# Performance work log

Measured on AMD Instinct MI355X. Metric: run time of the kernel, lower is better.

## Reference

```python
import jax, jax.numpy as jnp
import numpy as np

EPS = 1e-5

def _layer_norm(x, gamma, beta):
    mu = jnp.mean(x, axis=-1, keepdims=True)
    var = jnp.var(x, axis=-1, keepdims=True)
    return (x - mu) * jax.lax.rsqrt(var + EPS) * gamma + beta

def setup_inputs() -> dict:
    key = jax.random.key(0)
    ks = jax.random.split(key, 4)
    B, T, D, H = 16, 2048, 1024, 1024
    s_in = 1.0 / np.sqrt(D)
    return {
        "x": jax.random.normal(ks[0], (B, T, D), dtype=jnp.float32),
        "c": jnp.zeros((B, H), dtype=jnp.float32),
        "W_lt": jax.random.uniform(ks[1], (H, D), jnp.float32, -s_in, s_in),
        "W_g": jax.random.uniform(ks[2], (2 * H, D), jnp.float32, -s_in, s_in),
        "b_g": jnp.zeros((2 * H,), dtype=jnp.float32),
        "gamma_g": jnp.ones((2 * H,), dtype=jnp.float32),
        "beta_g": jnp.zeros((2 * H,), dtype=jnp.float32),
        "gamma_a": jnp.ones((H,), dtype=jnp.float32),
        "beta_a": jnp.zeros((H,), dtype=jnp.float32),
    }

def reference(x, c, W_lt, W_g, b_g, gamma_g, beta_g, gamma_a, beta_a):
    H = W_lt.shape[0]
    # x: [B,T,D]
    x_tilde = jnp.einsum("btd,hd->bth", x, W_lt)            # [B,T,H]
    gate = jax.nn.sigmoid(_layer_norm(jnp.einsum("btd,gd->btg", x, W_g) + b_g, gamma_g, beta_g))
    f = gate[:, :, :H]                                        # forget gate [B,T,H]
    r = gate[:, :, H:]                                        # reset gate  [B,T,H]
    new_data = (1.0 - f) * x_tilde

    def step(c_prev, ft_nd):
        f_t, nd_t = ft_nd
        c_t = f_t * c_prev + nd_t
        return c_t, c_t

    # scan over time: move T to leading axis
    c_final, all_c = jax.lax.scan(step, c, (jnp.swapaxes(f, 0, 1), jnp.swapaxes(new_data, 0, 1)))
    all_c = jnp.swapaxes(all_c, 0, 1)                         # [B,T,H]
    h = r * jax.nn.sigmoid(_layer_norm(all_c, gamma_a, beta_a)) + (1.0 - r) * x
    return (h, c_final)
```

## Files before the change

### kernel.cpp

```cpp
#include <hip/hip_runtime.h>
#include <stdint.h>

typedef unsigned short u16;
typedef u16 us8 __attribute__((ext_vector_type(8)));
typedef uint32_t u32x8 __attribute__((ext_vector_type(8)));
typedef __bf16 bf16x8 __attribute__((ext_vector_type(8)));
typedef float f32x4 __attribute__((ext_vector_type(4)));

#define BB 16
#define TT 2048
#define HH 1024
#define MM 32768
#define NN 3072
#define KK 1024
#define NT 16

__device__ __forceinline__ float b2f(u16 u) {
    union { uint32_t i; float f; } v; v.i = ((uint32_t)u) << 16; return v.f;
}
__device__ __forceinline__ u16 f2b(float f) {
    union { uint32_t i; float f; } v; v.f = f;
    uint32_t r = v.i + 0x7fffu + ((v.i >> 16) & 1u);
    return (u16)(r >> 16);
}
__device__ __forceinline__ float sigm(float z) {
    return 1.f / (1.f + __expf(-z));
}
__device__ __forceinline__ void load_lds16(const u16* g, u16* l) {
    __builtin_amdgcn_global_load_lds(
        (const __attribute__((address_space(1))) void*)g,
        (__attribute__((address_space(3))) void*)l, 16, 0, 0);
}
__device__ __forceinline__ f32x4 mf(bf16x8 a, bf16x8 b, f32x4 c) {
    return __builtin_amdgcn_mfma_f32_16x16x32_bf16(a, b, c, 0, 0, 0);
}

__global__ __launch_bounds__(256) void k_cvt(const float* __restrict__ x,
                                             const float* __restrict__ wlt,
                                             const float* __restrict__ wg,
                                             u16* __restrict__ xb,
                                             u16* __restrict__ wb) {
    long i = (long)(blockIdx.x * 256 + threadIdx.x) * 8;
    const float* s;
    u16* o;
    if (i < 33554432L) { s = x + i; o = xb + i; }
    else {
        long j = i - 33554432L;
        s = (j < 1048576L) ? (wlt + j) : (wg + (j - 1048576L));
        o = wb + j;
    }
    float4 a = *(const float4*)(s);
    float4 b = *(const float4*)(s + 4);
    us8 r;
    r[0] = f2b(a.x); r[1] = f2b(a.y); r[2] = f2b(a.z); r[3] = f2b(a.w);
    r[4] = f2b(b.x); r[5] = f2b(b.y); r[6] = f2b(b.z); r[7] = f2b(b.w);
    *(us8*)o = r;
}

__global__ __launch_bounds__(512, 2) void k_gemm(const u16* __restrict__ A,
                                                 const u16* __restrict__ W,
                                                 u16* __restrict__ Y) {
    __shared__ u16 As[2 * 16384];
    __shared__ u16 Bs[2 * 16384];
    const int tid = threadIdx.x;
    const int lane = tid & 63;
    const int w = tid >> 6;
    const int wm = w >> 2;
    const int wn = w & 3;
    const int q = lane >> 4;
    const int l16 = lane & 15;
    const int bx = blockIdx.x;
    const int by = blockIdx.y;

    const int slog = ((tid & 7) ^ ((tid >> 3) & 7)) << 3;
    const u16* aS = A + (size_t)(by * 256 + (tid >> 3)) * KK + slog;
    const u16* bS = W + (size_t)(bx * 256 + ((tid >> 8) << 6) + ((tid >> 3) & 31)) * KK + slog;
    u16* aD = As + w * 512;
    u16* bD = Bs + w * 512;

    load_lds16(aS,                aD);
    load_lds16(aS + 128 * KK,     aD + 4096);
    load_lds16(aS + 64 * KK,      aD + 8192);
    load_lds16(aS + 192 * KK,     aD + 12288);
    load_lds16(bS,                bD);
    load_lds16(bS + 128 * KK,     bD + 4096);
    load_lds16(bS + 32 * KK,      bD + 8192);
    load_lds16(bS + 160 * KK,     bD + 12288);
    load_lds16(aS + 64,           aD + 16384);
    load_lds16(aS + 64 + 128*KK,  aD + 16384 + 4096);
    load_lds16(aS + 64 + 64*KK,   aD + 16384 + 8192);
    load_lds16(aS + 64 + 192*KK,  aD + 16384 + 12288);
    load_lds16(bS + 64,           bD + 16384);
    load_lds16(bS + 64 + 128*KK,  bD + 16384 + 4096);
    load_lds16(bS + 64 + 32*KK,   bD + 16384 + 8192);
    load_lds16(bS + 64 + 160*KK,  bD + 16384 + 12288);

    const int key = l16 & 7;
    const int sA0 = ((q ^ key) << 3);
    const int sA1 = (((q ^ key) ^ 4) << 3);
    const int aB0 = wm * 4096 + l16 * 64 + sA0;
    const int aB1 = wm * 4096 + l16 * 64 + sA1;
    const int bB0 = wn * 2048 + l16 * 64 + sA0;
    const int bB1 = wn * 2048 + l16 * 64 + sA1;

    f32x4 zero = {0.f, 0.f, 0.f, 0.f};
    f32x4 acc[8][4];
#pragma unroll
    for (int i = 0; i < 8; ++i)
#pragma unroll
        for (int j = 0; j < 4; ++j) acc[i][j] = zero;
    bf16x8 aR[4][2], bR[4][2];

    asm volatile("s_waitcnt vmcnt(8)" ::: "memory");
    __builtin_amdgcn_sched_barrier(0);
    __builtin_amdgcn_s_barrier();
    asm volatile("" ::: "memory");

    for (int kt = 0; kt < NT; ++kt) {
        const int cb = (kt & 1) << 14;
        const int kc = (kt + 2) << 6;
#pragma unroll
        for (int i = 0; i < 4; ++i) {
            aR[i][0] = *(const bf16x8*)&As[cb + i * 1024 + aB0];
            aR[i][1] = *(const bf16x8*)&As[cb + i * 1024 + aB1];
        }
#pragma unroll
        for (int f = 0; f < 4; ++f) {
            bR[f][0] = *(const bf16x8*)&Bs[cb + (f >> 1) * 8192 + (f & 1) * 1024 + bB0];
            bR[f][1] = *(const bf16x8*)&Bs[cb + (f >> 1) * 8192 + (f & 1) * 1024 + bB1];
        }
        asm volatile("" ::: "memory");
        __builtin_amdgcn_s_barrier();
        asm volatile("s_waitcnt lgkmcnt(0)" ::: "memory");
        __builtin_amdgcn_sched_barrier(0);
        __builtin_amdgcn_s_setprio(1);
#pragma unroll
        for (int i = 0; i < 4; ++i)
#pragma unroll
            for (int f = 0; f < 2; ++f) {
                acc[i][f] = mf(aR[i][0], bR[f][0], acc[i][f]);
                acc[i][f] = mf(aR[i][1], bR[f][1], acc[i][f]);
            }
        __builtin_amdgcn_s_setprio(0);
        asm volatile("" ::: "memory");
        __builtin_amdgcn_s_barrier();
        asm volatile("" ::: "memory");
        if (kt < NT - 2) {
            load_lds16(aS + kc,            aD + cb);
            load_lds16(aS + kc + 128*KK,   aD + cb + 4096);
            load_lds16(bS + kc,            bD + cb);
            load_lds16(bS + kc + 128*KK,   bD + cb + 4096);
            load_lds16(bS + kc + 32*KK,    bD + cb + 8192);
            load_lds16(bS + kc + 160*KK,   bD + cb + 12288);
        }
        asm volatile("" ::: "memory");
        __builtin_amdgcn_s_barrier();
        __builtin_amdgcn_s_setprio(1);
#pragma unroll
        for (int i = 0; i < 4; ++i)
#pragma unroll
            for (int f = 2; f < 4; ++f) {
                acc[i][f] = mf(aR[i][0], bR[f][0], acc[i][f]);
                acc[i][f] = mf(aR[i][1], bR[f][1], acc[i][f]);
            }
        __builtin_amdgcn_s_setprio(0);
        asm volatile("" ::: "memory");
        __builtin_amdgcn_s_barrier();
        asm volatile("" ::: "memory");
#pragma unroll
        for (int i = 0; i < 4; ++i) {
            aR[i][0] = *(const bf16x8*)&As[cb + 8192 + i * 1024 + aB0];
            aR[i][1] = *(const bf16x8*)&As[cb + 8192 + i * 1024 + aB1];
        }
        asm volatile("" ::: "memory");
        __builtin_amdgcn_s_barrier();
        asm volatile("s_waitcnt lgkmcnt(0)" ::: "memory");
        __builtin_amdgcn_sched_barrier(0);
        __builtin_amdgcn_s_setprio(1);
#pragma unroll
        for (int i = 0; i < 4; ++i)
#pragma unroll
            for (int f = 0; f < 2; ++f) {
                acc[4 + i][f] = mf(aR[i][0], bR[f][0], acc[4 + i][f]);
                acc[4 + i][f] = mf(aR[i][1], bR[f][1], acc[4 + i][f]);
            }
        __builtin_amdgcn_s_setprio(0);
        asm volatile("" ::: "memory");
        __builtin_amdgcn_s_barrier();
        asm volatile("" ::: "memory");
        if (kt < NT - 2) {
            load_lds16(aS + kc + 64*KK,    aD + cb + 8192);
            load_lds16(aS + kc + 192*KK,   aD + cb + 12288);
        }
        asm volatile("" ::: "memory");
        __builtin_amdgcn_s_barrier();
        __builtin_amdgcn_s_setprio(1);
#pragma unroll
        for (int i = 0; i < 4; ++i)
#pragma unroll
            for (int f = 2; f < 4; ++f) {
                acc[4 + i][f] = mf(aR[i][0], bR[f][0], acc[4 + i][f]);
                acc[4 + i][f] = mf(aR[i][1], bR[f][1], acc[4 + i][f]);
            }
        __builtin_amdgcn_s_setprio(0);
        if (kt < NT - 2) { asm volatile("s_waitcnt vmcnt(8)" ::: "memory"); }
        else             { asm volatile("s_waitcnt vmcnt(0)" ::: "memory"); }
        __builtin_amdgcn_sched_barrier(0);
        __builtin_amdgcn_s_barrier();
        asm volatile("" ::: "memory");
    }

#pragma unroll
    for (int fm = 0; fm < 8; ++fm) {
#pragma unroll
        for (int rg = 0; rg < 4; ++rg) {
            const int row = by * 256 + wm * 128 + fm * 16 + q * 4 + rg;
            u16* yp = Y + (size_t)row * NN + bx * 256 + wn * 64 + l16;
#pragma unroll
            for (int fn = 0; fn < 4; ++fn) yp[fn * 16] = f2b(acc[fm][fn][rg]);
        }
    }
}

__global__ __launch_bounds__(256) void k_lnsig(const u16* __restrict__ Y,
                                               const float* __restrict__ bg,
                                               const float* __restrict__ gg,
                                               const float* __restrict__ bt,
                                               uint32_t* __restrict__ FN,
                                               u16* __restrict__ R) {
    const int row = blockIdx.x;
    const int t = threadIdx.x;
    const u16* yr = Y + (size_t)row * 3072;
    us8 gv = *(const us8*)(yr + 1024 + t * 8);
    float z[8];
    float s = 0.f, s2 = 0.f;
#pragma unroll
    for (int k = 0; k < 8; k++) {
        z[k] = b2f(gv[k]) + bg[t * 8 + k];
        s += z[k];
        s2 += z[k] * z[k];
    }
#pragma unroll
    for (int m = 1; m < 64; m <<= 1) {
        s += __shfl_xor(s, m);
        s2 += __shfl_xor(s2, m);
    }
    __shared__ float red[8];
    if ((t & 63) == 0) { red[t >> 6] = s; red[(t >> 6) + 4] = s2; }
    __syncthreads();
    s = red[0] + red[1] + red[2] + red[3];
    s2 = red[4] + red[5] + red[6] + red[7];
    const float mu = s * (1.f / 2048.f);
    const float inv = rsqrtf(s2 * (1.f / 2048.f) - mu * mu + 1e-5f);
    float gate[8];
#pragma unroll
    for (int k = 0; k < 8; k++)
        gate[k] = sigm((z[k] - mu) * inv * gg[t * 8 + k] + bt[t * 8 + k]);
    if (t < 128) {
        us8 xt = *(const us8*)(yr + t * 8);
        u32x8 fn;
#pragma unroll
        for (int k = 0; k < 8; k++) {
            u16 fb = f2b(gate[k]);
            u16 nb = f2b((1.f - gate[k]) * b2f(xt[k]));
            fn[k] = (uint32_t)fb | ((uint32_t)nb << 16);
        }
        *(u32x8*)(FN + (size_t)row * 1024 + t * 8) = fn;
    } else {
        us8 ro;
#pragma unroll
        for (int k = 0; k < 8; k++) ro[k] = f2b(gate[k]);
        *(us8*)(R + (size_t)row * 1024 + (t - 128) * 8) = ro;
    }
}

__global__ __launch_bounds__(256) void k_scan1(const uint32_t* __restrict__ FN,
                                               float2* __restrict__ agg) {
    int u = blockIdx.x * 256 + threadIdx.x;
    int h2 = u & 511;
    int chunk = (u >> 9) & 31;
    int b = u >> 14;
    size_t base = (size_t)(b * 2048 + chunk * 64) * 1024 + h2 * 2;
    float F0 = 1.f, N0 = 0.f, F1 = 1.f, N1 = 0.f;
#pragma unroll 4
    for (int i = 0; i < 64; i++) {
        uint2 v = *(const uint2*)(FN + base + (size_t)i * 1024);
        float f0 = b2f((u16)(v.x & 0xffffu)), n0 = b2f((u16)(v.x >> 16));
        float f1 = b2f((u16)(v.y & 0xffffu)), n1 = b2f((u16)(v.y >> 16));
        N0 = fmaf(f0, N0, n0); F0 *= f0;
        N1 = fmaf(f1, N1, n1); F1 *= f1;
    }
    float4 o = {F0, N0, F1, N1};
    *(float4*)&agg[(size_t)(b * 32 + chunk) * 1024 + h2 * 2] = o;
}

__global__ __launch_bounds__(256) void k_scan2(const float2* __restrict__ agg,
                                               const float* __restrict__ c0,
                                               float* __restrict__ P) {
    int u = blockIdx.x * 256 + threadIdx.x;
    int b = u >> 10, h = u & 1023;
    float c = c0[u];
#pragma unroll 4
    for (int k = 0; k < 32; k++) {
        size_t idx = (size_t)(b * 32 + k) * 1024 + h;
        P[idx] = c;
        float2 fn = agg[idx];
        c = fmaf(fn.x, c, fn.y);
    }
}

__global__ __launch_bounds__(512) void k_scanout(const uint32_t* __restrict__ FN,
                                                 const float* __restrict__ P,
                                                 const u16* __restrict__ R,
                                                 const u16* __restrict__ xb,
                                                 const float* __restrict__ ga,
                                                 const float* __restrict__ ba,
                                                 float* __restrict__ out,
                                                 float* __restrict__ cfin) {
    __shared__ float2 red[2][8];
    const int t = threadIdx.x;
    const int b = blockIdx.x >> 5, chunk = blockIdx.x & 31;
    const int h = t * 2;
    const int w = t >> 6, lane = t & 63;
    float2 cp = *(const float2*)&P[(size_t)(b * 32 + chunk) * 1024 + h];
    float c0 = cp.x, c1 = cp.y;
    const float g0 = ga[h], g1 = ga[h + 1];
    const float be0 = ba[h], be1 = ba[h + 1];
    const size_t base = (size_t)(b * 2048 + chunk * 64) * 1024 + h;
#pragma unroll 2
    for (int i = 0; i < 64; i++) {
        const size_t ro = base + (size_t)i * 1024;
        uint2 fn = *(const uint2*)(FN + ro);
        uint32_t rv = *(const uint32_t*)(R + ro);
        uint32_t xv = *(const uint32_t*)(xb + ro);
        c0 = fmaf(b2f((u16)(fn.x & 0xffffu)), c0, b2f((u16)(fn.x >> 16)));
        c1 = fmaf(b2f((u16)(fn.y & 0xffffu)), c1, b2f((u16)(fn.y >> 16)));
        float s = c0 + c1, s2 = c0 * c0 + c1 * c1;
#pragma unroll
        for (int m = 1; m < 64; m <<= 1) {
            s += __shfl_xor(s, m);
            s2 += __shfl_xor(s2, m);
        }
        const int p = i & 1;
        if (lane == 0) red[p][w] = make_float2(s, s2);
        __syncthreads();
        s = 0.f; s2 = 0.f;
#pragma unroll
        for (int k = 0; k < 8; k++) { float2 v = red[p][k]; s += v.x; s2 += v.y; }
        const float mu = s * (1.f / 1024.f);
        const float inv = rsqrtf(s2 * (1.f / 1024.f) - mu * mu + 1e-5f);
        const float sg0 = sigm((c0 - mu) * inv * g0 + be0);
        const float sg1 = sigm((c1 - mu) * inv * g1 + be1);
        const float r0 = b2f((u16)(rv & 0xffffu)), r1 = b2f((u16)(rv >> 16));
        const float x0 = b2f((u16)(xv & 0xffffu)), x1 = b2f((u16)(xv >> 16));
        float2 ho = {r0 * sg0 + (1.f - r0) * x0, r1 * sg1 + (1.f - r1) * x1};
        *(float2*)(out + ro) = ho;
    }
    if (chunk == 31) *(float2*)(cfin + b * 1024 + h) = make_float2(c0, c1);
}

extern "C" void kernel_launch(void* const* d_in, const int* in_sizes, int n_in,
                              void* d_out, int out_size, void* d_ws, size_t ws_size,
                              hipStream_t stream) {
    const float* x   = (const float*)d_in[0];
    const float* c0  = (const float*)d_in[1];
    const float* wlt = (const float*)d_in[2];
    const float* wg  = (const float*)d_in[3];
    const float* bg  = (const float*)d_in[4];
    const float* gg  = (const float*)d_in[5];
    const float* btg = (const float*)d_in[6];
    const float* ga  = (const float*)d_in[7];
    const float* ba  = (const float*)d_in[8];
    float* out = (float*)d_out;

    char* ws = (char*)d_ws;
    u16* xb      = (u16*)(ws);
    u16* wb      = (u16*)(ws + 67108864);
    u16* y       = (u16*)(ws + 73400320);
    uint32_t* FN = (uint32_t*)(ws + 274726912);
    u16* R       = (u16*)(ws + 408944640);
    float2* agg  = (float2*)(ws + 476053504);
    float* P     = (float*)(ws + 480247808);

    k_cvt<<<17920, 256, 0, stream>>>(x, wlt, wg, xb, wb);
    k_gemm<<<dim3(NN / 256, MM / 256), 512, 0, stream>>>(xb, wb, y);
    k_lnsig<<<32768, 256, 0, stream>>>(y, bg, gg, btg, FN, R);
    k_scan1<<<1024, 256, 0, stream>>>(FN, agg);
    k_scan2<<<64, 256, 0, stream>>>(agg, c0, P);
    k_scanout<<<512, 512, 0, stream>>>(FN, P, R, xb, ga, ba, out,
                                       out + (size_t)33554432);
}
```

Baseline: 669.1 us.

## Software-pipeline LDS fragment reads across GEMM k-halves with register double buffering

Restructures the GEMM main loop so LDS reads of the next k-half fragments (aX/aY, b0/b1) are issued before the MFMAs on the current fragments. It prefetches the first tile before the loop and peels the last iteration into an epilogue. It also drops several explicit lgkmcnt(0) waits and barriers. The aim is to hide LDS latency behind MFMA work and cut stalls from synchronisation, at the cost of more live registers and a more intricate schedule that relies on the compiler inserting correct waits.

After: 663.6 us. Within noise of the previous version (-0.8%).

```diff
diff --git a/kernel.cpp b/kernel.cpp
--- a/kernel.cpp
+++ b/kernel.cpp
@@ -34,6 +34,7 @@
 __device__ __forceinline__ f32x4 mf(bf16x8 a, bf16x8 b, f32x4 c) {
     return __builtin_amdgcn_mfma_f32_16x16x32_bf16(a, b, c, 0, 0, 0);
 }
+#define MEMBAR() asm volatile("" ::: "memory")
 
 __global__ __launch_bounds__(256) void k_cvt(const float* __restrict__ x,
                                              const float* __restrict__ wlt,
@@ -109,42 +110,38 @@
     for (int i = 0; i < 8; ++i)
 #pragma unroll
         for (int j = 0; j < 4; ++j) acc[i][j] = zero;
-    bf16x8 aR[4][2], bR[4][2];
+    bf16x8 aX[4], aY[4], b0[4], b1[4];
 
     asm volatile("s_waitcnt vmcnt(8)" ::: "memory");
     __builtin_amdgcn_sched_barrier(0);
     __builtin_amdgcn_s_barrier();
-    asm volatile("" ::: "memory");
-
-    for (int kt = 0; kt < NT; ++kt) {
+    MEMBAR();
+
+#pragma unroll
+    for (int i = 0; i < 4; ++i) aX[i] = *(const bf16x8*)&As[i * 1024 + aB0];
+#pragma unroll
+    for (int f = 0; f < 4; ++f)
+        b0[f] = *(const bf16x8*)&Bs[(f >> 1) * 8192 + (f & 1) * 1024 + bB0];
+
+    for (int kt = 0; kt < NT - 1; ++kt) {
         const int cb = (kt & 1) << 14;
+        const int nb = cb ^ 16384;
         const int kc = (kt + 2) << 6;
 #pragma unroll
-        for (int i = 0; i < 4; ++i) {
-            aR[i][0] = *(const bf16x8*)&As[cb + i * 1024 + aB0];
-            aR[i][1] = *(const bf16x8*)&As[cb + i * 1024 + aB1];
-        }
-#pragma unroll
-        for (int f = 0; f < 4; ++f) {
-            bR[f][0] = *(const bf16x8*)&Bs[cb + (f >> 1) * 8192 + (f & 1) * 1024 + bB0];
-            bR[f][1] = *(const bf16x8*)&Bs[cb + (f >> 1) * 8192 + (f & 1) * 1024 + bB1];
-        }
-        asm volatile("" ::: "memory");
+        for (int i = 0; i < 4; ++i) aY[i] = *(const bf16x8*)&As[cb + i * 1024 + aB1];
+#pragma unroll
+        for (int f = 0; f < 4; ++f)
+            b1[f] = *(const bf16x8*)&Bs[cb + (f >> 1) * 8192 + (f & 1) * 1024 + bB1];
+        __builtin_amdgcn_sched_barrier(0);
+        __builtin_amdgcn_s_setprio(1);
+#pragma unroll
+        for (int i = 0; i < 4; ++i)
+#pragma unroll
+            for (int f = 0; f < 4; ++f) acc[i][f] = mf(aX[i], b0[f], acc[i][f]);
+        __builtin_amdgcn_s_setprio(0);
+        MEMBAR();
         __builtin_amdgcn_s_barrier();
-        asm volatile("s_waitcnt lgkmcnt(0)" ::: "memory");
-        __builtin_amdgcn_sched_barrier(0);
-        __builtin_amdgcn_s_setprio(1);
-#pragma unroll
-        for (int i = 0; i < 4; ++i)
-#pragma unroll
-            for (int f = 0; f < 2; ++f) {
-                acc[i][f] = mf(aR[i][0], bR[f][0], acc[i][f]);
-                acc[i][f] = mf(aR[i][1], bR[f][1], acc[i][f]);
-            }
-        __builtin_amdgcn_s_setprio(0);
-        asm volatile("" ::: "memory");
-        __builtin_amdgcn_s_barrier();
-        asm volatile("" ::: "memory");
+        MEMBAR();
         if (kt < NT - 2) {
             load_lds16(aS + kc,            aD + cb);
             load_lds16(aS + kc + 128*KK,   aD + cb + 4096);
@@ -153,61 +150,89 @@
             load_lds16(bS + kc + 32*KK,    bD + cb + 8192);
             load_lds16(bS + kc + 160*KK,   bD + cb + 12288);
         }
-        asm volatile("" ::: "memory");
+#pragma unroll
+        for (int i = 0; i < 4; ++i)
+            aX[i] = *(const bf16x8*)&As[cb + 8192 + i * 1024 + aB0];
+        __builtin_amdgcn_sched_barrier(0);
+        __builtin_amdgcn_s_setprio(1);
+#pragma unroll
+        for (int i = 0; i < 4; ++i)
+#pragma unroll
+            for (int f = 0; f < 4; ++f) acc[i][f] = mf(aY[i], b1[f], acc[i][f]);
+        __builtin_amdgcn_s_setprio(0);
+#pragma unroll
+        for (int i = 0; i < 4; ++i)
+            aY[i] = *(const bf16x8*)&As[cb + 8192 + i * 1024 + aB1];
+        __builtin_amdgcn_sched_barrier(0);
+        __builtin_amdgcn_s_setprio(1);
+#pragma unroll
+        for (int i = 0; i < 4; ++i)
+#pragma unroll
+            for (int f = 0; f < 4; ++f) acc[4 + i][f] = mf(aX[i], b0[f], acc[4 + i][f]);
+        __builtin_amdgcn_s_setprio(0);
+        MEMBAR();
         __builtin_amdgcn_s_barrier();
-        __builtin_amdgcn_s_setprio(1);
-#pragma unroll
-        for (int i = 0; i < 4; ++i)
-#pragma unroll
-            for (int f = 2; f < 4; ++f) {
-                acc[i][f] = mf(aR[i][0], bR[f][0], acc[i][f]);
-                acc[i][f] = mf(aR[i][1], bR[f][1], acc[i][f]);
-            }
-        __builtin_amdgcn_s_setprio(0);
-        asm volatile("" ::: "memory");
-        __builtin_amdgcn_s_barrier();
-        asm volatile("" ::: "memory");
-#pragma unroll
-        for (int i = 0; i < 4; ++i) {
-            aR[i][0] = *(const bf16x8*)&As[cb + 8192 + i * 1024 + aB0];
-            aR[i][1] = *(const bf16x8*)&As[cb + 8192 + i * 1024 + aB1];
-        }
-        asm volatile("" ::: "memory");
-        __builtin_amdgcn_s_barrier();
-        asm volatile("s_waitcnt lgkmcnt(0)" ::: "memory");
-        __builtin_amdgcn_sched_barrier(0);
-        __builtin_amdgcn_s_setprio(1);
-#pragma unroll
-        for (int i = 0; i < 4; ++i)
-#pragma unroll
-            for (int f = 0; f < 2; ++f) {
-                acc[4 + i][f] = mf(aR[i][0], bR[f][0], acc[4 + i][f]);
-                acc[4 + i][f] = mf(aR[i][1], bR[f][1], acc[4 + i][f]);
-            }
-        __builtin_amdgcn_s_setprio(0);
-        asm volatile("" ::: "memory");
-        __builtin_amdgcn_s_barrier();
-        asm volatile("" ::: "memory");
+        MEMBAR();
         if (kt < NT - 2) {
             load_lds16(aS + kc + 64*KK,    aD + cb + 8192);
             load_lds16(aS + kc + 192*KK,   aD + cb + 12288);
+            asm volatile("s_waitcnt vmcnt(8)" ::: "memory");
+        } else {
+            asm volatile("s_waitcnt vmcnt(0)" ::: "memory");
         }
-        asm volatile("" ::: "memory");
+        __builtin_amdgcn_sched_barrier(0);
         __builtin_amdgcn_s_barrier();
+        MEMBAR();
+#pragma unroll
+        for (int i = 0; i < 4; ++i) aX[i] = *(const bf16x8*)&As[nb + i * 1024 + aB0];
+#pragma unroll
+        for (int f = 0; f < 4; ++f)
+            b0[f] = *(const bf16x8*)&Bs[nb + (f >> 1) * 8192 + (f & 1) * 1024 + bB0];
+        __builtin_amdgcn_sched_barrier(0);
         __builtin_amdgcn_s_setprio(1);
 #pragma unroll
         for (int i = 0; i < 4; ++i)
 #pragma unroll
-            for (int f = 2; f < 4; ++f) {
-                acc[4 + i][f] = mf(aR[i][0], bR[f][0], acc[4 + i][f]);
-                acc[4 + i][f] = mf(aR[i][1], bR[f][1], acc[4 + i][f]);
-            }
+            for (int f = 0; f < 4; ++f) acc[4 + i][f] = mf(aY[i], b1[f], acc[4 + i][f]);
         __builtin_amdgcn_s_setprio(0);
-        if (kt < NT - 2) { asm volatile("s_waitcnt vmcnt(8)" ::: "memory"); }
-        else             { asm volatile("s_waitcnt vmcnt(0)" ::: "memory"); }
-        __builtin_amdgcn_sched_barrier(0);
+        MEMBAR();
         __builtin_amdgcn_s_barrier();
-        asm volatile("" ::: "memory");
+        MEMBAR();
+    }
+
+    {
+        const int cb = 16384;
+#pragma unroll
+        for (int i = 0; i < 4; ++i) aY[i] = *(const bf16x8*)&As[cb + i * 1024 + aB1];
+#pragma unroll
+        for (int f = 0; f < 4; ++f)
+            b1[f] = *(const bf16x8*)&Bs[cb + (f >> 1) * 8192 + (f & 1) * 1024 + bB1];
+        __builtin_amdgcn_sched_barrier(0);
+#pragma unroll
+        for (int i = 0; i < 4; ++i)
+#pragma unroll
+            for (int f = 0; f < 4; ++f) acc[i][f] = mf(aX[i], b0[f], acc[i][f]);
+#pragma unroll
+        for (int i = 0; i < 4; ++i)
+            aX[i] = *(const bf16x8*)&As[cb + 8192 + i * 1024 + aB0];
+        __builtin_amdgcn_sched_barrier(0);
+#pragma unroll
+        for (int i = 0; i < 4; ++i)
+#pragma unroll
+            for (int f = 0; f < 4; ++f) acc[i][f] = mf(aY[i], b1[f], acc[i][f]);
+#pragma unroll
+        for (int i = 0; i < 4; ++i)
+            aY[i] = *(const bf16x8*)&As[cb + 8192 + i * 1024 + aB1];
+        __builtin_amdgcn_sched_barrier(0);
+#pragma unroll
+        for (int i = 0; i < 4; ++i)
+#pragma unroll
+            for (int f = 0; f < 4; ++f) acc[4 + i][f] = mf(aX[i], b0[f], acc[4 + i][f]);
+        __builtin_amdgcn_sched_barrier(0);
+#pragma unroll
+        for (int i = 0; i < 4; ++i)
+#pragma unroll
+            for (int f = 0; f < 4; ++f) acc[4 + i][f] = mf(aY[i], b1[f], acc[4 + i][f]);
     }
 
 #pragma unroll
```
